# Kernel optimization log

Measured on AMD Instinct MI355X. Metric: run time of the kernel, lower is better.

## Reference

```python
import jax, jax.numpy as jnp
import numpy as np

EPS = 1e-8
K_KNN = 20

def vn_lin(W, x):
    # W: [Cout, Cin], x: [B, Cin, 3, ...] -> [B, Cout, 3, ...]
    return jnp.einsum('oi,bi...->bo...', W, x)

def vn_relu(Wd, x):
    # VNLeakyReLU with negative_slope=0, share_nonlinearity=False
    d = jnp.einsum('oi,bi...->bo...', Wd, x)
    dot = jnp.sum(x * d, axis=2, keepdims=True)   # sum over 3-vector axis
    dsq = jnp.sum(d * d, axis=2, keepdims=True) + EPS
    return jnp.where(dot >= 0, x, x - (dot / dsq) * d)

def graph_feature_cross(p, k):
    # p: [B, N, 3] -> feat: [B, 3, 3, N, k]
    xx = jnp.sum(p * p, axis=-1)                       # [B,N]
    inner = jnp.einsum('bnd,bmd->bnm', p, p)           # [B,N,N]
    neg_dist = 2.0 * inner - xx[:, :, None] - xx[:, None, :]
    idx = jax.lax.top_k(neg_dist, k)[1]                # [B,N,k] nearest neighbors
    nbrs = jax.vmap(lambda pb, ib: pb[ib])(p, idx)     # [B,N,k,3]
    xr = jnp.broadcast_to(p[:, :, None, :], nbrs.shape)
    cross = jnp.cross(nbrs, xr)                        # [B,N,k,3]
    feat = jnp.stack([nbrs - xr, xr, cross], axis=3)   # [B,N,k,3(ch),3(vec)]
    return jnp.transpose(feat, (0, 3, 4, 1, 2))        # [B,3,3,N,k]

def setup_inputs() -> dict:
    key = jax.random.key(0)
    ks = jax.random.split(key, 9)
    B, N = 4, 2048
    H = 128           # hidden_dim // 3
    C_IN = 2 * H      # 256
    CC = 128          # c_dim // 3
    s_in = 1.0 / np.sqrt(C_IN)
    s_h = 1.0 / np.sqrt(H)
    return {
        'p': jax.random.normal(ks[0], (B, N, 3), dtype=jnp.float32),
        'fc_pos_W': jax.random.normal(ks[1], (C_IN, 3), dtype=jnp.float32) / np.sqrt(3.0),
        'blk_d0': jax.random.normal(ks[2], (5, C_IN, C_IN), dtype=jnp.float32) * s_in,
        'blk_W0': jax.random.normal(ks[3], (5, H, C_IN), dtype=jnp.float32) * s_in,
        'blk_d1': jax.random.normal(ks[4], (5, H, H), dtype=jnp.float32) * s_h,
        'blk_W1': jax.random.normal(ks[5], (5, H, H), dtype=jnp.float32) * s_h,
        'blk_Ws': jax.random.normal(ks[6], (5, H, C_IN), dtype=jnp.float32) * s_in,
        'fc_c_W': jax.random.normal(ks[7], (CC, H), dtype=jnp.float32) * s_h,
        'act_d': jax.random.normal(ks[8], (H, H), dtype=jnp.float32) * s_h,
    }

def reference(p, fc_pos_W, blk_d0, blk_W0, blk_d1, blk_W1, blk_Ws, fc_c_W, act_d):
    feat = graph_feature_cross(p, K_KNN)          # [B,3,3,N,k]
    x = vn_lin(fc_pos_W, feat)                    # [B,256,3,N,k]
    net = jnp.mean(x, axis=-1)                    # mean_pool over k -> [B,256,3,N]

    def block(i, x):
        h = vn_lin(blk_W0[i], vn_relu(blk_d0[i], x))
        dx = vn_lin(blk_W1[i], vn_relu(blk_d1[i], h))
        return vn_lin(blk_Ws[i], x) + dx          # shortcut (size_in != size_out)

    net = block(0, net)                           # [B,128,3,N]
    for i in range(1, 5):
        pooled = jnp.broadcast_to(jnp.mean(net, axis=3, keepdims=True), net.shape)
        net = block(i, jnp.concatenate([net, pooled], axis=1))
    net = jnp.mean(net, axis=3)                   # [B,128,3]
    c = vn_lin(fc_c_W, vn_relu(act_d, net))       # [B,128,3]
    return c.reshape(c.shape[0], -1)              # [B,384]
```

## Files before the change

### kernel.cpp

```cpp
#include <hip/hip_runtime.h>
#include <math.h>

#define N_PTS 2048
#define K_NN  20
#define K_D   10
#define WTOT  819200
#define NM_REP 8
#define NM_STRIDE 1536
#define NM_BLK (NM_REP*NM_STRIDE)
#define NBLK 256
#define BPB  64
#define ROWS 96
#define LDS_BYTES (2*ROWS*264*2)

typedef unsigned short u16;
typedef unsigned int   u32;
typedef _Float16 f16;
using half8   = __attribute__((ext_vector_type(8))) _Float16;
using floatx4 = __attribute__((ext_vector_type(4))) float;

__device__ __forceinline__ void split2h(float v, f16& h, f16& l) {
    h = (f16)v;
    l = (f16)((v - (float)h) * 1024.0f);
}

__device__ __forceinline__ float neg_dist(float4 q2, float4 c) {
    return fmaf(q2.x, c.x, fmaf(q2.y, c.y, fmaf(q2.z, c.z, -q2.w))) - c.w;
}

__global__ __launch_bounds__(256) void prep_kernel(
    const float* __restrict__ pts, float* __restrict__ m_out,
    const float* __restrict__ bd0, const float* __restrict__ bW0,
    const float* __restrict__ bd1, const float* __restrict__ bW1,
    const float* __restrict__ bWs, u16* __restrict__ Wswz,
    float* __restrict__ nm_acc)
{
    __shared__ float4 sp[N_PTS];
    if (blockIdx.x >= 1024) {
        int i = (blockIdx.x - 1024) * 256 + threadIdx.x;
        if (i >= WTOT) return;
        if (i < 5*NM_BLK + 32) nm_acc[i] = 0.f;
        float v; int base, K, local;
        if (i < 327680)      { int rel = i;          base = (rel/65536)*65536;            local = rel%65536; K = 256; v = bd0[rel]; }
        else if (i < 491520) { int rel = i - 327680; base = 327680 + (rel/32768)*32768;   local = rel%32768; K = 256; v = bW0[rel]; }
        else if (i < 573440) { int rel = i - 491520; base = 491520 + (rel/16384)*16384;   local = rel%16384; K = 128; v = bd1[rel]; }
        else if (i < 655360) { int rel = i - 573440; base = 573440 + (rel/16384)*16384;   local = rel%16384; K = 128; v = bW1[rel]; }
        else                 { int rel = i - 655360; base = 655360 + (rel/32768)*32768;   local = rel%32768; K = 256; v = bWs[rel]; }
        int m = local / K, k = local % K;
        int NKF = K >> 5;
        int mf = m >> 4, r = m & 15;
        int kf = k >> 5, q = (k >> 3) & 3, ii = k & 7;
        int lane = q*16 + r;
        int dst = base + ((mf*NKF + kf)*64 + lane)*8 + ii;
        f16 h, l; split2h(v, h, l);
        f16* W = (f16*)Wswz;
        W[dst] = h; W[WTOT + dst] = l;
        return;
    }

    const int b     = blockIdx.x >> 8;
    const int qbase = (blockIdx.x & 255) << 3;
    const int ql    = threadIdx.x >> 5;
    const int sl    = threadIdx.x & 31;
    const float* pb = pts + (size_t)b * N_PTS * 3;
    for (int i = threadIdx.x; i < N_PTS; i += 256) {
        float x = pb[i*3+0], y = pb[i*3+1], z = pb[i*3+2];
        sp[i] = make_float4(x, y, z, x*x + y*y + z*z);
    }
    __syncthreads();

    const int n = qbase + ql;
    const float4 q = sp[n];
    const float4 q2 = make_float4(2.f*q.x, 2.f*q.y, 2.f*q.z, q.w);

    float t[K_D];
#pragma unroll
    for (int s = 0; s < K_D; ++s) t[s] = -INFINITY;

    for (int j = 0; j < N_PTS/32; ++j) {
        float4 c = sp[j*32 + sl];
        float v = neg_dist(q2, c);
#pragma unroll
        for (int s = 0; s < K_D; ++s) {
            float nx = (s < K_D-1) ? t[s+1] : INFINITY;
            t[s] = fminf(fmaxf(t[s], v), nx);
        }
    }

    float head = t[K_D-1];
    float T = -INFINITY;
#pragma unroll 1
    for (int e = 0; e < K_NN; ++e) {
        float v = head; int w = sl;
#pragma unroll
        for (int off = 1; off < 32; off <<= 1) {
            float vo = __shfl_xor(v, off);
            int   wo = __shfl_xor(w, off);
            bool take = (vo > v) || (vo == v && wo < w);
            v = take ? vo : v;
            w = take ? wo : w;
        }
        T = v;
        if (w == sl) {
#pragma unroll
            for (int s = K_D-1; s > 0; --s) t[s] = t[s-1];
            t[0] = -INFINITY;
            head = t[K_D-1];
        }
    }

    float sx = 0.f, sy = 0.f, sz = 0.f;
    for (int j = 0; j < N_PTS/32; ++j) {
        float4 c = sp[j*32 + sl];
        float v = neg_dist(q2, c);
        if (v >= T) { sx += c.x; sy += c.y; sz += c.z; }
    }
#pragma unroll
    for (int off = 1; off < 32; off <<= 1) {
        sx += __shfl_xor(sx, off);
        sy += __shfl_xor(sy, off);
        sz += __shfl_xor(sz, off);
    }
    if (sl == 0) {
        const float inv = 1.0f / (float)K_NN;
        const int pt = b * N_PTS + n;
        m_out[pt*3+0] = sx * inv;
        m_out[pt*3+1] = sy * inv;
        m_out[pt*3+2] = sz * inv;
    }
}

template<int MF, int JF, int NK, int BS>
__device__ __forceinline__ void run_gemm_hi(
    const f16* __restrict__ Whi, size_t aoff,
    int kf0, int kf1, const f16* Blds, int lane,
    floatx4 (&acc)[MF][JF])
{
    const int l15 = lane & 15;
    const int lq8 = (lane >> 4) * 8;
    half8 Aa[MF], Ab[MF];

    auto loada = [&](half8 (&dst)[MF], int kf) {
#pragma unroll
        for (int fm = 0; fm < MF; ++fm)
            dst[fm] = *(const half8*)(Whi + aoff + (size_t)fm*NK*512 + (size_t)kf*512 + (size_t)lane*8);
    };
    auto step = [&](half8 (&af)[MF], int kf) {
        half8 bq[JF];
#pragma unroll
        for (int fj = 0; fj < JF; ++fj)
            bq[fj] = *(const half8*)&Blds[(fj*16 + l15)*BS + kf*32 + lq8];
#pragma unroll
        for (int fm = 0; fm < MF; ++fm)
#pragma unroll
            for (int fj = 0; fj < JF; ++fj)
                acc[fm][fj] = __builtin_amdgcn_mfma_f32_16x16x32_f16(af[fm], bq[fj], acc[fm][fj], 0, 0, 0);
    };

    loada(Aa, kf0);
#pragma unroll 1
    for (int kf = kf0; kf < kf1; kf += 2) {
        loada(Ab, kf + 1);
        step(Aa, kf);
        if (kf + 2 < kf1) loada(Aa, kf + 2);
        step(Ab, kf + 1);
    }
}

template<int MF, int JF, int NK, int BS>
__device__ __forceinline__ void run_gemm_split(
    const f16* __restrict__ Whi, const f16* __restrict__ Wlo, size_t aoff,
    int kf0, int kf1, const f16* Blds, int lane,
    floatx4 (&acc)[MF][JF], floatx4 (&accL)[MF][JF])
{
    const int l15 = lane & 15;
    const int lq8 = (lane >> 4) * 8;
    half8 Aa[2*MF], Ab[2*MF];

    auto loada = [&](half8 (&dst)[2*MF], int kf) {
#pragma unroll
        for (int fm = 0; fm < MF; ++fm) {
            size_t fo = aoff + (size_t)fm*NK*512 + (size_t)kf*512 + (size_t)lane*8;
            dst[fm*2+0] = *(const half8*)(Whi + fo);
            dst[fm*2+1] = *(const half8*)(Wlo + fo);
        }
    };
    auto step = [&](half8 (&af)[2*MF], int kf) {
        half8 bq[JF];
#pragma unroll
        for (int fj = 0; fj < JF; ++fj)
            bq[fj] = *(const half8*)&Blds[(fj*16 + l15)*BS + kf*32 + lq8];
#pragma unroll
        for (int fm = 0; fm < MF; ++fm)
#pragma unroll
            for (int fj = 0; fj < JF; ++fj) {
                acc[fm][fj]  = __builtin_amdgcn_mfma_f32_16x16x32_f16(af[fm*2+0], bq[fj], acc[fm][fj], 0, 0, 0);
                accL[fm][fj] = __builtin_amdgcn_mfma_f32_16x16x32_f16(af[fm*2+1], bq[fj], accL[fm][fj], 0, 0, 0);
            }
    };

    loada(Aa, kf0);
#pragma unroll 1
    for (int kf = kf0; kf < kf1; kf += 2) {
        loada(Ab, kf + 1);
        step(Aa, kf);
        if (kf + 2 < kf1) loada(Aa, kf + 2);
        step(Ab, kf + 1);
    }
}

template<int BS>
__device__ __forceinline__ void run_gemm_merged(
    const f16* __restrict__ Whi, const f16* __restrict__ Wlo,
    size_t aoff1, size_t aoff4,
    int kf0, int kf1, const f16* Blds, int lane,
    floatx4 (&acc1)[4][3], floatx4 (&acc4)[2][3], floatx4 (&accL4)[2][3])
{
    const int l15 = lane & 15;
    const int lq8 = (lane >> 4) * 8;
    half8 Aa1[4], Ab1[4], Aa4[4], Ab4[4];

    auto loada = [&](half8 (&d1)[4], half8 (&d4)[4], int kf) {
#pragma unroll
        for (int fm = 0; fm < 4; ++fm)
            d1[fm] = *(const half8*)(Whi + aoff1 + (size_t)fm*8*512 + (size_t)kf*512 + (size_t)lane*8);
#pragma unroll
        for (int fm = 0; fm < 2; ++fm) {
            size_t fo = aoff4 + (size_t)fm*8*512 + (size_t)kf*512 + (size_t)lane*8;
            d4[fm*2+0] = *(const half8*)(Whi + fo);
            d4[fm*2+1] = *(const half8*)(Wlo + fo);
        }
    };
    auto step = [&](half8 (&a1)[4], half8 (&a4)[4], int kf) {
        half8 bq[3];
#pragma unroll
        for (int fj = 0; fj < 3; ++fj)
            bq[fj] = *(const half8*)&Blds[(fj*16 + l15)*BS + kf*32 + lq8];
#pragma unroll
        for (int fm = 0; fm < 4; ++fm)
#pragma unroll
            for (int fj = 0; fj < 3; ++fj)
                acc1[fm][fj] = __builtin_amdgcn_mfma_f32_16x16x32_f16(a1[fm], bq[fj], acc1[fm][fj], 0, 0, 0);
#pragma unroll
        for (int fm = 0; fm < 2; ++fm)
#pragma unroll
            for (int fj = 0; fj < 3; ++fj) {
                acc4[fm][fj]  = __builtin_amdgcn_mfma_f32_16x16x32_f16(a4[fm*2+0], bq[fj], acc4[fm][fj], 0, 0, 0);
                accL4[fm][fj] = __builtin_amdgcn_mfma_f32_16x16x32_f16(a4[fm*2+1], bq[fj], accL4[fm][fj], 0, 0, 0);
            }
    };

    loada(Aa1, Aa4, kf0);
#pragma unroll 1
    for (int kf = kf0; kf < kf1; kf += 2) {
        loada(Ab1, Ab4, kf + 1);
        step(Aa1, Aa4, kf);
        if (kf + 2 < kf1) loada(Aa1, Aa4, kf + 2);
        step(Ab1, Ab4, kf + 1);
    }
}

__device__ __forceinline__ uint2 pack_res(floatx4 a, floatx4 aL) {
    u16 hh[4];
#pragma unroll
    for (int r = 0; r < 4; ++r) {
        f16 hv = (f16)(a[r] + aL[r] * (1.0f/1024.0f));
        hh[r] = *(u16*)&hv;
    }
    uint2 pv;
    pv.x = (u32)hh[0] | ((u32)hh[1] << 16);
    pv.y = (u32)hh[2] | ((u32)hh[3] << 16);
    return pv;
}

__device__ __forceinline__ uint2 pack_hi(floatx4 a) {
    u16 hh[4];
#pragma unroll
    for (int r = 0; r < 4; ++r) {
        f16 hv = (f16)a[r];
        hh[r] = *(u16*)&hv;
    }
    uint2 pv;
    pv.x = (u32)hh[0] | ((u32)hh[1] << 16);
    pv.y = (u32)hh[2] | ((u32)hh[3] << 16);
    return pv;
}

__global__ __launch_bounds__(512, 2) void resnet_kernel(
    const u16* __restrict__ Wswz,
    const float* __restrict__ pts, const float* __restrict__ m_buf,
    const float* __restrict__ fcW,
    float* __restrict__ nm_acc, int* __restrict__ cnt,
    const float* __restrict__ act_d, const float* __restrict__ fc_c,
    float* __restrict__ out)
{
    extern __shared__ char smem_raw[];
    f16*   X  = (f16*)smem_raw;
    f16*   Yd = X + ROWS*264;
    float* YC = (float*)Yd;

    const int tid   = threadIdx.x;
    const int bB    = blockIdx.x / BPB;
    const int lane  = tid & 63;
    const int wv    = tid >> 6;
    const int mwave = wv >> 1;
    const int ncol  = wv & 1;
    const f16* Whi = (const f16*)Wswz;
    const f16* Wlo = Whi + WTOT;

#pragma unroll 1
    for (int st = 0; st < 5; ++st) {
        const int offD0 = st*65536;
        const int offW0 = 327680 + st*32768;
        const int offD1 = 491520 + st*16384;
        const int offW1 = 573440 + st*16384;
        const int offWs = 655360 + st*32768;

        if (st == 0) {
            float* Hf = YC;
            const int ptbase = blockIdx.x * 32;
            for (int i = tid; i < 768; i += 512) Hf[i] = fcW[i];
            if (tid < 192) Hf[768 + tid] = (tid < 96) ? pts[ptbase*3 + tid]
                                                      : m_buf[ptbase*3 + tid - 96];
            __syncthreads();
#pragma unroll 1
            for (int it = 0; it < 6; ++it) {
                int idx = tid + 512*it;
                int r = idx >> 5;
                int cg = idx & 31;
                int l = r / 3, v = r - l*3;
                float pv0[3] = {Hf[768+l*3], Hf[768+l*3+1], Hf[768+l*3+2]};
                float mv0[3] = {Hf[864+l*3], Hf[864+l*3+1], Hf[864+l*3+2]};
                int v1 = (v==2) ? 0 : v+1;
                int v2 = (v==0) ? 2 : v-1;
                float av = mv0[v] - pv0[v];
                float bv = pv0[v];
                float cv = mv0[v1]*pv0[v2] - mv0[v2]*pv0[v1];
                half8 o;
#pragma unroll
                for (int k = 0; k < 8; ++k) {
                    int ch = cg*8 + k;
                    o[k] = (f16)(Hf[ch*3+0]*av + Hf[ch*3+1]*bv + Hf[ch*3+2]*cv);
                }
                *(half8*)&X[r*264 + cg*8] = o;
            }
            __syncthreads();
        }

        floatx4 acc1[4][3];
        floatx4 acc4[2][3], accL4[2][3];
#pragma unroll
        for (int a = 0; a < 4; ++a)
#pragma unroll
            for (int b = 0; b < 3; ++b) acc1[a][b] = (floatx4){0,0,0,0};
#pragma unroll
        for (int a = 0; a < 2; ++a)
#pragma unroll
            for (int b = 0; b < 3; ++b) { acc4[a][b] = (floatx4){0,0,0,0}; accL4[a][b] = (floatx4){0,0,0,0}; }

        const size_t aoff1 = (size_t)offD0 + (size_t)mwave*16384;
        const size_t aoff4 = (size_t)offWs + (size_t)mwave*8192;

        if (st == 0) {
            run_gemm_merged<264>(Whi, Wlo, aoff1, aoff4, 0, 8,
                                 X + ncol*48*264, lane, acc1, acc4, accL4);
        } else {
            run_gemm_merged<264>(Whi, Wlo, aoff1, aoff4, 0, 4,
                                 X + ncol*48*264, lane, acc1, acc4, accL4);

            if (tid == 0) {
                while (__hip_atomic_load(&cnt[(st-1)*4+bB], __ATOMIC_RELAXED, __HIP_MEMORY_SCOPE_AGENT) < BPB)
                    __builtin_amdgcn_s_sleep(8);
            }
            __syncthreads();

            float* nmSp = nm_acc + (size_t)(st-1)*NM_BLK;
            f16* nmT = Yd;
            if (tid < 384) {
                int v = tid >> 7, ch = tid & 127;
                float sum = 0.f;
#pragma unroll
                for (int rep = 0; rep < NM_REP; ++rep)
                    sum += __hip_atomic_load(nmSp + rep*NM_STRIDE + (bB*3+v)*128 + ch,
                                             __ATOMIC_RELAXED, __HIP_MEMORY_SCOPE_AGENT);
                nmT[tid] = (f16)(sum * (1.0f/2048.0f));
            }
            __syncthreads();
#pragma unroll 1
            for (int idx = tid; idx < 1536; idx += 512) {
                int r = idx >> 4;
                int cg = (idx & 15) + 16;
                int v = r % 3;
                *(half8*)&X[r*264 + cg*8] = *(const half8*)&nmT[v*128 + (cg-16)*8];
            }
            __syncthreads();

            run_gemm_merged<264>(Whi, Wlo, aoff1, aoff4, 4, 8,
                                 X + ncol*48*264, lane, acc1, acc4, accL4);
        }

#pragma unroll
        for (int fm = 0; fm < 4; ++fm)
#pragma unroll
            for (int fj = 0; fj < 3; ++fj) {
                int mloc = mwave*64 + fm*16 + (lane>>4)*4;
                int jl   = ncol*48 + fj*16 + (lane & 15);
                *(uint2*)&Yd[jl*264 + mloc] = pack_hi(acc1[fm][fj]);
            }
        __syncthreads();

#pragma unroll 1
        for (int it = 0; it < 2; ++it) {
            int idx = tid + 512*it;
            int l = idx >> 5, cg = idx & 31;
            half8 xa = *(const half8*)&X[(l*3+0)*264 + cg*8];
            half8 xb = *(const half8*)&X[(l*3+1)*264 + cg*8];
            half8 xc = *(const half8*)&X[(l*3+2)*264 + cg*8];
            half8 da = *(const half8*)&Yd[(l*3+0)*264 + cg*8];
            half8 db = *(const half8*)&Yd[(l*3+1)*264 + cg*8];
            half8 dc = *(const half8*)&Yd[(l*3+2)*264 + cg*8];
            half8 ya, yb, yc;
#pragma unroll
            for (int k = 0; k < 8; ++k) {
                float x0 = (float)xa[k], x1 = (float)xb[k], x2 = (float)xc[k];
                float d0 = (float)da[k], d1 = (float)db[k], d2 = (float)dc[k];
                float dot = x0*d0 + x1*d1 + x2*d2;
                float y0, y1, y2;
                if (dot >= 0.f) { y0 = x0; y1 = x1; y2 = x2; }
                else {
                    float dsq = d0*d0 + d1*d1 + d2*d2 + 1e-8f;
                    float sc = dot / dsq;
                    y0 = x0 - sc*d0; y1 = x1 - sc*d1; y2 = x2 - sc*d2;
                }
                ya[k] = (f16)y0; yb[k] = (f16)y1; yc[k] = (f16)y2;
            }
            *(half8*)&Yd[(l*3+0)*264 + cg*8] = ya;
            *(half8*)&Yd[(l*3+1)*264 + cg*8] = yb;
            *(half8*)&Yd[(l*3+2)*264 + cg*8] = yc;
        }
        __syncthreads();

        {
            floatx4 acc[2][3], accL[2][3];
#pragma unroll
            for (int a = 0; a < 2; ++a)
#pragma unroll
                for (int b = 0; b < 3; ++b) { acc[a][b] = (floatx4){0,0,0,0}; accL[a][b] = (floatx4){0,0,0,0}; }
            run_gemm_split<2,3,8,264>(Whi, Wlo, (size_t)offW0 + (size_t)mwave*8192, 0, 8,
                                      Yd + ncol*48*264, lane, acc, accL);
#pragma unroll
            for (int fm = 0; fm < 2; ++fm)
#pragma unroll
                for (int fj = 0; fj < 3; ++fj) {
                    int mloc = mwave*32 + fm*16 + (lane>>4)*4;
                    int jl   = ncol*48 + fj*16 + (lane & 15);
                    *(uint2*)&X[jl*136 + mloc] = pack_res(acc[fm][fj], accL[fm][fj]);
                }
        }
        __syncthreads();

        {
            floatx4 acc[2][3];
#pragma unroll
            for (int a = 0; a < 2; ++a)
#pragma unroll
                for (int b = 0; b < 3; ++b) acc[a][b] = (floatx4){0,0,0,0};
            run_gemm_hi<2,3,4,136>(Whi, (size_t)offD1 + (size_t)mwave*4096, 0, 4,
                                   X + ncol*48*136, lane, acc);
#pragma unroll
            for (int fm = 0; fm < 2; ++fm)
#pragma unroll
                for (int fj = 0; fj < 3; ++fj) {
                    int mloc = mwave*32 + fm*16 + (lane>>4)*4;
                    int jl   = ncol*48 + fj*16 + (lane & 15);
                    *(uint2*)&Yd[jl*136 + mloc] = pack_hi(acc[fm][fj]);
                }
        }
        __syncthreads();

        {
            int l = tid >> 4, cg = tid & 15;
            half8 xa = *(const half8*)&X[(l*3+0)*136 + cg*8];
            half8 xb = *(const half8*)&X[(l*3+1)*136 + cg*8];
            half8 xc = *(const half8*)&X[(l*3+2)*136 + cg*8];
            half8 da = *(const half8*)&Yd[(l*3+0)*136 + cg*8];
            half8 db = *(const half8*)&Yd[(l*3+1)*136 + cg*8];
            half8 dc = *(const half8*)&Yd[(l*3+2)*136 + cg*8];
            half8 ya, yb, yc;
#pragma unroll
            for (int k = 0; k < 8; ++k) {
                float x0 = (float)xa[k], x1 = (float)xb[k], x2 = (float)xc[k];
                float d0 = (float)da[k], d1 = (float)db[k], d2 = (float)dc[k];
                float dot = x0*d0 + x1*d1 + x2*d2;
                float y0, y1, y2;
                if (dot >= 0.f) { y0 = x0; y1 = x1; y2 = x2; }
                else {
                    float dsq = d0*d0 + d1*d1 + d2*d2 + 1e-8f;
                    float sc = dot / dsq;
                    y0 = x0 - sc*d0; y1 = x1 - sc*d1; y2 = x2 - sc*d2;
                }
                ya[k] = (f16)y0; yb[k] = (f16)y1; yc[k] = (f16)y2;
            }
            *(half8*)&X[(l*3+0)*136 + cg*8] = ya;
            *(half8*)&X[(l*3+1)*136 + cg*8] = yb;
            *(half8*)&X[(l*3+2)*136 + cg*8] = yc;
        }
        __syncthreads();

        run_gemm_split<2,3,4,136>(Whi, Wlo, (size_t)offW1 + (size_t)mwave*4096, 0, 4,
                                  X + ncol*48*136, lane, acc4, accL4);
        __syncthreads();

#pragma unroll
        for (int fm = 0; fm < 2; ++fm)
#pragma unroll
            for (int fj = 0; fj < 3; ++fj) {
                int mloc = mwave*32 + fm*16 + (lane>>4)*4;
                int jl   = ncol*48 + fj*16 + (lane & 15);
                floatx4 res;
#pragma unroll
                for (int r = 0; r < 4; ++r) res[r] = acc4[fm][fj][r] + accL4[fm][fj][r] * (1.0f/1024.0f);
                *(uint2*)&X[jl*264 + mloc] = pack_res(acc4[fm][fj], accL4[fm][fj]);
                *(floatx4*)&YC[jl*132 + mloc] = res;
            }
        __syncthreads();

        const int rsel = (blockIdx.x & (NM_REP-1)) * NM_STRIDE;
        float* nmS = nm_acc + (size_t)st*NM_BLK;
        if (tid < 384) {
            int v = tid >> 7, ch = tid & 127;
            float sum = 0.f;
#pragma unroll 1
            for (int pt = 0; pt < 32; ++pt) sum += YC[(pt*3+v)*132 + ch];
            atomicAdd(nmS + rsel + (bB*3+v)*128 + ch, sum);
        }
        asm volatile("s_waitcnt vmcnt(0)" ::: "memory");
        __syncthreads();
        if (tid == 0)
            __hip_atomic_fetch_add(&cnt[st*4+bB], 1, __ATOMIC_RELAXED, __HIP_MEMORY_SCOPE_AGENT);
    }

    if (blockIdx.x < 4) {
        const int b = blockIdx.x;
        if (tid == 0) {
            while (__hip_atomic_load(&cnt[16+b], __ATOMIC_RELAXED, __HIP_MEMORY_SCOPE_AGENT) < BPB)
                __builtin_amdgcn_s_sleep(8);
        }
        __syncthreads();
        float* xs = (float*)smem_raw;
        float* ys = xs + 384;
        const float* nm4 = nm_acc + (size_t)4*NM_BLK;
        if (tid < 128) {
            int c = tid;
            float s0 = 0.f, s1 = 0.f, s2 = 0.f;
#pragma unroll
            for (int rep = 0; rep < NM_REP; ++rep) {
                s0 += __hip_atomic_load(nm4 + rep*NM_STRIDE + (b*3+0)*128 + c, __ATOMIC_RELAXED, __HIP_MEMORY_SCOPE_AGENT);
                s1 += __hip_atomic_load(nm4 + rep*NM_STRIDE + (b*3+1)*128 + c, __ATOMIC_RELAXED, __HIP_MEMORY_SCOPE_AGENT);
                s2 += __hip_atomic_load(nm4 + rep*NM_STRIDE + (b*3+2)*128 + c, __ATOMIC_RELAXED, __HIP_MEMORY_SCOPE_AGENT);
            }
            xs[c*3+0] = s0 * (1.0f/2048.0f);
            xs[c*3+1] = s1 * (1.0f/2048.0f);
            xs[c*3+2] = s2 * (1.0f/2048.0f);
        }
        __syncthreads();
        if (tid < 128) {
            int c = tid;
            float d0 = 0.f, d1 = 0.f, d2 = 0.f;
            for (int i = 0; i < 128; ++i) {
                float w = act_d[c*128 + i];
                d0 = fmaf(w, xs[i*3+0], d0);
                d1 = fmaf(w, xs[i*3+1], d1);
                d2 = fmaf(w, xs[i*3+2], d2);
            }
            float x0 = xs[c*3+0], x1 = xs[c*3+1], x2 = xs[c*3+2];
            float dot = x0*d0 + x1*d1 + x2*d2;
            float y0, y1, y2;
            if (dot >= 0.f) { y0 = x0; y1 = x1; y2 = x2; }
            else {
                float dsq = d0*d0 + d1*d1 + d2*d2 + 1e-8f;
                float sc = dot / dsq;
                y0 = x0 - sc*d0; y1 = x1 - sc*d1; y2 = x2 - sc*d2;
            }
            ys[c*3+0] = y0; ys[c*3+1] = y1; ys[c*3+2] = y2;
        }
        __syncthreads();
        if (tid < 128) {
            int c = tid;
            float o0 = 0.f, o1 = 0.f, o2 = 0.f;
            for (int i = 0; i < 128; ++i) {
                float w = fc_c[c*128 + i];
                o0 = fmaf(w, ys[i*3+0], o0);
                o1 = fmaf(w, ys[i*3+1], o1);
                o2 = fmaf(w, ys[i*3+2], o2);
            }
            out[b*384 + c*3 + 0] = o0;
            out[b*384 + c*3 + 1] = o1;
            out[b*384 + c*3 + 2] = o2;
        }
    }
}

extern "C" void kernel_launch(void* const* d_in, const int* in_sizes, int n_in,
                              void* d_out, int out_size, void* d_ws, size_t ws_size,
                              hipStream_t stream)
{
    const float* p      = (const float*)d_in[0];
    const float* fc_pos = (const float*)d_in[1];
    const float* bd0    = (const float*)d_in[2];
    const float* bW0    = (const float*)d_in[3];
    const float* bd1    = (const float*)d_in[4];
    const float* bW1    = (const float*)d_in[5];
    const float* bWs    = (const float*)d_in[6];
    const float* fc_c   = (const float*)d_in[7];
    const float* act_d  = (const float*)d_in[8];
    float* out = (float*)d_out;

    char* w = (char*)d_ws;
    float* m_buf  = (float*)w;  w += 98304;
    float* nm_acc = (float*)w;  w += (size_t)5*NM_BLK*4;
    int*   cnt    = (int*)w;    w += 128;
    u16*   Wswz   = (u16*)w;    w += (size_t)2*WTOT*2;

    static bool attr_set = false;
    if (!attr_set) {
        hipFuncSetAttribute((const void*)resnet_kernel,
                            hipFuncAttributeMaxDynamicSharedMemorySize, LDS_BYTES);
        attr_set = true;
    }

    prep_kernel<<<dim3(1024 + 3200), dim3(256), 0, stream>>>(
        p, m_buf, bd0, bW0, bd1, bW1, bWs, Wswz, nm_acc);

    resnet_kernel<<<dim3(NBLK), dim3(512), LDS_BYTES, stream>>>(
        Wswz, p, m_buf, fc_pos, nm_acc, cnt, act_d, fc_c, out);

    (void)in_sizes; (void)n_in; (void)out_size; (void)ws_size;
}
```

Measured before the change: 214.3 us.

## Double resnet block size to 1024 threads, halving per-wave GEMM row tiles

Launches the resnet kernel with 1024 threads (16 waves) instead of 512, so each wave computes half as many output-row fragments in every GEMM stage. Loop strides and elementwise stages are adjusted to match. The goal is more waves per CU to hide weight-load latency with fewer registers per wave. The cost is that each block issues its own weight loads across twice as many waves, plus more barrier overhead. Launch bounds of (1024,4) may be impossible to meet given the LDS use per block.

Measured after the change: 227.9 us. 1.06x slower.

```diff
diff --git a/kernel.cpp b/kernel.cpp
--- a/kernel.cpp
+++ b/kernel.cpp
@@ -214,40 +214,35 @@
     const f16* __restrict__ Whi, const f16* __restrict__ Wlo,
     size_t aoff1, size_t aoff4,
     int kf0, int kf1, const f16* Blds, int lane,
-    floatx4 (&acc1)[4][3], floatx4 (&acc4)[2][3], floatx4 (&accL4)[2][3])
+    floatx4 (&acc1)[2][3], floatx4 (&acc4)[1][3], floatx4 (&accL4)[1][3])
 {
     const int l15 = lane & 15;
     const int lq8 = (lane >> 4) * 8;
-    half8 Aa1[4], Ab1[4], Aa4[4], Ab4[4];
-
-    auto loada = [&](half8 (&d1)[4], half8 (&d4)[4], int kf) {
-#pragma unroll
-        for (int fm = 0; fm < 4; ++fm)
+    half8 Aa1[2], Ab1[2], Aa4[2], Ab4[2];
+
+    auto loada = [&](half8 (&d1)[2], half8 (&d4)[2], int kf) {
+#pragma unroll
+        for (int fm = 0; fm < 2; ++fm)
             d1[fm] = *(const half8*)(Whi + aoff1 + (size_t)fm*8*512 + (size_t)kf*512 + (size_t)lane*8);
-#pragma unroll
-        for (int fm = 0; fm < 2; ++fm) {
-            size_t fo = aoff4 + (size_t)fm*8*512 + (size_t)kf*512 + (size_t)lane*8;
-            d4[fm*2+0] = *(const half8*)(Whi + fo);
-            d4[fm*2+1] = *(const half8*)(Wlo + fo);
-        }
+        size_t fo = aoff4 + (size_t)kf*512 + (size_t)lane*8;
+        d4[0] = *(const half8*)(Whi + fo);
+        d4[1] = *(const half8*)(Wlo + fo);
     };
-    auto step = [&](half8 (&a1)[4], half8 (&a4)[4], int kf) {
+    auto step = [&](half8 (&a1)[2], half8 (&a4)[2], int kf) {
         half8 bq[3];
 #pragma unroll
         for (int fj = 0; fj < 3; ++fj)
             bq[fj] = *(const half8*)&Blds[(fj*16 + l15)*BS + kf*32 + lq8];
 #pragma unroll
-        for (int fm = 0; fm < 4; ++fm)
+        for (int fm = 0; fm < 2; ++fm)
 #pragma unroll
             for (int fj = 0; fj < 3; ++fj)
                 acc1[fm][fj] = __builtin_amdgcn_mfma_f32_16x16x32_f16(a1[fm], bq[fj], acc1[fm][fj], 0, 0, 0);
 #pragma unroll
-        for (int fm = 0; fm < 2; ++fm)
-#pragma unroll
-            for (int fj = 0; fj < 3; ++fj) {
-                acc4[fm][fj]  = __builtin_amdgcn_mfma_f32_16x16x32_f16(a4[fm*2+0], bq[fj], acc4[fm][fj], 0, 0, 0);
-                accL4[fm][fj] = __builtin_amdgcn_mfma_f32_16x16x32_f16(a4[fm*2+1], bq[fj], accL4[fm][fj], 0, 0, 0);
-            }
+        for (int fj = 0; fj < 3; ++fj) {
+            acc4[0][fj]  = __builtin_amdgcn_mfma_f32_16x16x32_f16(a4[0], bq[fj], acc4[0][fj], 0, 0, 0);
+            accL4[0][fj] = __builtin_amdgcn_mfma_f32_16x16x32_f16(a4[1], bq[fj], accL4[0][fj], 0, 0, 0);
+        }
     };
 
     loada(Aa1, Aa4, kf0);
@@ -286,7 +281,7 @@
     return pv;
 }
 
-__global__ __launch_bounds__(512, 2) void resnet_kernel(
+__global__ __launch_bounds__(1024, 4) void resnet_kernel(
     const u16* __restrict__ Wswz,
     const float* __restrict__ pts, const float* __restrict__ m_buf,
     const float* __restrict__ fcW,
@@ -319,13 +314,13 @@
         if (st == 0) {
             float* Hf = YC;
             const int ptbase = blockIdx.x * 32;
-            for (int i = tid; i < 768; i += 512) Hf[i] = fcW[i];
+            if (tid < 768) Hf[tid] = fcW[tid];
             if (tid < 192) Hf[768 + tid] = (tid < 96) ? pts[ptbase*3 + tid]
                                                       : m_buf[ptbase*3 + tid - 96];
             __syncthreads();
 #pragma unroll 1
-            for (int it = 0; it < 6; ++it) {
-                int idx = tid + 512*it;
+            for (int it = 0; it < 3; ++it) {
+                int idx = tid + 1024*it;
                 int r = idx >> 5;
                 int cg = idx & 31;
                 int l = r / 3, v = r - l*3;
@@ -347,19 +342,17 @@
             __syncthreads();
         }
 
-        floatx4 acc1[4][3];
-        floatx4 acc4[2][3], accL4[2][3];
-#pragma unroll
-        for (int a = 0; a < 4; ++a)
+        floatx4 acc1[2][3];
+        floatx4 acc4[1][3], accL4[1][3];
+#pragma unroll
+        for (int a = 0; a < 2; ++a)
 #pragma unroll
             for (int b = 0; b < 3; ++b) acc1[a][b] = (floatx4){0,0,0,0};
 #pragma unroll
-        for (int a = 0; a < 2; ++a)
-#pragma unroll
-            for (int b = 0; b < 3; ++b) { acc4[a][b] = (floatx4){0,0,0,0}; accL4[a][b] = (floatx4){0,0,0,0}; }
-
-        const size_t aoff1 = (size_t)offD0 + (size_t)mwave*16384;
-        const size_t aoff4 = (size_t)offWs + (size_t)mwave*8192;
+        for (int b = 0; b < 3; ++b) { acc4[0][b] = (floatx4){0,0,0,0}; accL4[0][b] = (floatx4){0,0,0,0}; }
+
+        const size_t aoff1 = (size_t)offD0 + (size_t)mwave*8192;
+        const size_t aoff4 = (size_t)offWs + (size_t)mwave*4096;
 
         if (st == 0) {
             run_gemm_merged<264>(Whi, Wlo, aoff1, aoff4, 0, 8,
@@ -387,7 +380,7 @@
             }
             __syncthreads();
 #pragma unroll 1
-            for (int idx = tid; idx < 1536; idx += 512) {
+            for (int idx = tid; idx < 1536; idx += 1024) {
                 int r = idx >> 4;
                 int cg = (idx & 15) + 16;
                 int v = r % 3;
@@ -400,19 +393,17 @@
         }
 
 #pragma unroll
-        for (int fm = 0; fm < 4; ++fm)
+        for (int fm = 0; fm < 2; ++fm)
 #pragma unroll
             for (int fj = 0; fj < 3; ++fj) {
-                int mloc = mwave*64 + fm*16 + (lane>>4)*4;
+                int mloc = mwave*32 + fm*16 + (lane>>4)*4;
                 int jl   = ncol*48 + fj*16 + (lane & 15);
                 *(uint2*)&Yd[jl*264 + mloc] = pack_hi(acc1[fm][fj]);
             }
         __syncthreads();
 
-#pragma unroll 1
-        for (int it = 0; it < 2; ++it) {
-            int idx = tid + 512*it;
-            int l = idx >> 5, cg = idx & 31;
+        {
+            int l = tid >> 5, cg = tid & 31;
             half8 xa = *(const half8*)&X[(l*3+0)*264 + cg*8];
             half8 xb = *(const half8*)&X[(l*3+1)*264 + cg*8];
             half8 xc = *(const half8*)&X[(l*3+2)*264 + cg*8];
@@ -441,44 +432,36 @@
         __syncthreads();
 
         {
-            floatx4 acc[2][3], accL[2][3];
-#pragma unroll
-            for (int a = 0; a < 2; ++a)
-#pragma unroll
-                for (int b = 0; b < 3; ++b) { acc[a][b] = (floatx4){0,0,0,0}; accL[a][b] = (floatx4){0,0,0,0}; }
-            run_gemm_split<2,3,8,264>(Whi, Wlo, (size_t)offW0 + (size_t)mwave*8192, 0, 8,
+            floatx4 acc[1][3], accL[1][3];
+#pragma unroll
+            for (int b = 0; b < 3; ++b) { acc[0][b] = (floatx4){0,0,0,0}; accL[0][b] = (floatx4){0,0,0,0}; }
+            run_gemm_split<1,3,8,264>(Whi, Wlo, (size_t)offW0 + (size_t)mwave*4096, 0, 8,
                                       Yd + ncol*48*264, lane, acc, accL);
 #pragma unroll
-            for (int fm = 0; fm < 2; ++fm)
-#pragma unroll
-                for (int fj = 0; fj < 3; ++fj) {
-                    int mloc = mwave*32 + fm*16 + (lane>>4)*4;
-                    int jl   = ncol*48 + fj*16 + (lane & 15);
-                    *(uint2*)&X[jl*136 + mloc] = pack_res(acc[fm][fj], accL[fm][fj]);
-                }
+            for (int fj = 0; fj < 3; ++fj) {
+                int mloc = mwave*16 + (lane>>4)*4;
+                int jl   = ncol*48 + fj*16 + (lane & 15);
+                *(uint2*)&X[jl*136 + mloc] = pack_res(acc[0][fj], accL[0][fj]);
+            }
         }
         __syncthreads();
 
         {
-            floatx4 acc[2][3];
-#pragma unroll
-            for (int a = 0; a < 2; ++a)
-#pragma unroll
-                for (int b = 0; b < 3; ++b) acc[a][b] = (floatx4){0,0,0,0};
-            run_gemm_hi<2,3,4,136>(Whi, (size_t)offD1 + (size_t)mwave*4096, 0, 4,
+            floatx4 acc[1][3];
+#pragma unroll
+            for (int b = 0; b < 3; ++b) acc[0][b] = (floatx4){0,0,0,0};
+            run_gemm_hi<1,3,4,136>(Whi, (size_t)offD1 + (size_t)mwave*2048, 0, 4,
                                    X + ncol*48*136, lane, acc);
 #pragma unroll
-            for (int fm = 0; fm < 2; ++fm)
-#pragma unroll
-                for (int fj = 0; fj < 3; ++fj) {
-                    int mloc = mwave*32 + fm*16 + (lane>>4)*4;
-                    int jl   = ncol*48 + fj*16 + (lane & 15);
-                    *(uint2*)&Yd[jl*136 + mloc] = pack_hi(acc[fm][fj]);
-                }
-        }
-        __syncthreads();
-
-        {
+            for (int fj = 0; fj < 3; ++fj) {
+                int mloc = mwave*16 + (lane>>4)*4;
+                int jl   = ncol*48 + fj*16 + (lane & 15);
+                *(uint2*)&Yd[jl*136 + mloc] = pack_hi(acc[0][fj]);
+            }
+        }
+        __syncthreads();
+
+        if (tid < 512) {
             int l = tid >> 4, cg = tid & 15;
             half8 xa = *(const half8*)&X[(l*3+0)*136 + cg*8];
             half8 xb = *(const half8*)&X[(l*3+1)*136 + cg*8];
@@ -507,22 +490,20 @@
         }
         __syncthreads();
 
-        run_gemm_split<2,3,4,136>(Whi, Wlo, (size_t)offW1 + (size_t)mwave*4096, 0, 4,
+        run_gemm_split<1,3,4,136>(Whi, Wlo, (size_t)offW1 + (size_t)mwave*2048, 0, 4,
                                   X + ncol*48*136, lane, acc4, accL4);
         __syncthreads();
 
 #pragma unroll
-        for (int fm = 0; fm < 2; ++fm)
-#pragma unroll
-            for (int fj = 0; fj < 3; ++fj) {
-                int mloc = mwave*32 + fm*16 + (lane>>4)*4;
-                int jl   = ncol*48 + fj*16 + (lane & 15);
-                floatx4 res;
-#pragma unroll
-                for (int r = 0; r < 4; ++r) res[r] = acc4[fm][fj][r] + accL4[fm][fj][r] * (1.0f/1024.0f);
-                *(uint2*)&X[jl*264 + mloc] = pack_res(acc4[fm][fj], accL4[fm][fj]);
-                *(floatx4*)&YC[jl*132 + mloc] = res;
-            }
+        for (int fj = 0; fj < 3; ++fj) {
+            int mloc = mwave*16 + (lane>>4)*4;
+            int jl   = ncol*48 + fj*16 + (lane & 15);
+            floatx4 res;
+#pragma unroll
+            for (int r = 0; r < 4; ++r) res[r] = acc4[0][fj][r] + accL4[0][fj][r] * (1.0f/1024.0f);
+            *(uint2*)&X[jl*264 + mloc] = pack_res(acc4[0][fj], accL4[0][fj]);
+            *(floatx4*)&YC[jl*132 + mloc] = res;
+        }
         __syncthreads();
 
         const int rsel = (blockIdx.x & (NM_REP-1)) * NM_STRIDE;
@@ -632,7 +613,7 @@
     prep_kernel<<<dim3(1024 + 3200), dim3(256), 0, stream>>>(
         p, m_buf, bd0, bW0, bd1, bW1, bWs, Wswz, nm_acc);
 
-    resnet_kernel<<<dim3(NBLK), dim3(512), LDS_BYTES, stream>>>(
+    resnet_kernel<<<dim3(NBLK), dim3(1024), LDS_BYTES, stream>>>(
         Wswz, p, m_buf, fc_pos, nm_acc, cnt, act_d, fc_c, out);
 
     (void)in_sizes; (void)n_in; (void)out_size; (void)ws_size;
```
